# Kernel tuning notes

Measured on AMD Instinct MI355X. Metric: run time of the kernel, lower is better.

The kernel has to match this reference:

```python
import jax, jax.numpy as jnp
import numpy as np

# Constants from init_kwargs
DT = 0.01
NIV = 8          # energy_input_dim[1]
HID = 64         # hidden_dims[0]
FEAT = 501       # per-field microstructure feature length (501+501=1002)


def _lin(k, fin, fout):
    return jax.random.normal(k, (fin, fout), dtype=jnp.float32) / np.sqrt(fin)


def setup_inputs() -> dict:
    key = jax.random.key(0)
    ks = jax.random.split(key, 12)
    B, T = 8192, 512
    e = jax.random.normal(ks[0], (B, T, 1), dtype=jnp.float32) * 0.1
    e_dot = jax.random.normal(ks[1], (B, T, 1), dtype=jnp.float32) * 0.1
    # positive microstructure fields (code computes nu**-1 and E/nu**2)
    E = jax.random.uniform(ks[2], (B, FEAT), minval=0.5, maxval=2.0, dtype=jnp.float32)
    nu = jax.random.uniform(ks[3], (B, FEAT), minval=0.5, maxval=2.0, dtype=jnp.float32)
    return {
        "e": e, "e_dot": e_dot, "E": E, "nu": nu,
        # EnergyFunction.B : Linear(1002,64) -> ReLU -> Linear(64,niv)
        "Bw1": _lin(ks[4], 2 * FEAT, HID), "Bb1": jnp.zeros((HID,), jnp.float32),
        "Bw2": _lin(ks[5], HID, NIV), "Bb2": jnp.zeros((NIV,), jnp.float32),
        # InverseDissipationPotential.beta : Linear(1002,64)->Softplus->Linear(64,niv)->Softplus
        "bw1": _lin(ks[6], 2 * FEAT, HID), "bb1": jnp.zeros((HID,), jnp.float32),
        "bw2": _lin(ks[7], HID, NIV), "bb2": jnp.zeros((NIV,), jnp.float32),
    }


def reference(e, e_dot, E, nu, Bw1, Bb1, Bw2, Bb2, bw1, bb1, bw2, bb2):
    # --- microstructure encoder (TrueFeatures) ---
    nu_p = 1.0 / jnp.mean(1.0 / nu, axis=1, keepdims=True)                 # [B,1]
    E_p = jnp.mean(E / nu ** 2, axis=1, keepdims=True) * nu_p ** 2         # [B,1]
    m = jnp.concatenate([E, nu], axis=-1)                                  # [B,1002]

    # Time-invariant MLP coefficients (hoisted out of the time loop)
    Bm = jax.nn.relu(m @ Bw1 + Bb1) @ Bw2 + Bb2                            # [B,NIV]
    beta = jax.nn.softplus(jax.nn.softplus(m @ bw1 + bb1) @ bw2 + bb2)     # [B,NIV]
    Bsum = jnp.sum(Bm, axis=-1, keepdims=True)                             # [B,1]

    B_, niv = Bm.shape
    xi0 = jnp.zeros((B_, niv), dtype=e.dtype)

    def step(xi, inp):
        u, p = inp                                                          # [B,1],[B,1]
        # Analytic gradients of L = sum_{b,k} Bm_bk * (0.5*E' u^2 + 0.5*(u-xi_k)^2 + 0.5*sum_j xi_j^2)
        du = u - xi                                                         # [B,NIV]
        grad_u = Bsum * E_p * u + jnp.sum(Bm * du, axis=-1, keepdims=True)  # [B,1] (s_eq)
        grad_v = -Bm * du + Bsum * xi                                       # [B,NIV] (d)
        q = -grad_v
        # Analytic gradients of potential = -0.5*nu' p^2 + 0.5*sum(beta*q^2)
        grad_p = -nu_p * p                                                  # [B,1] (s_neq)
        grad_q = beta * q                                                   # [B,NIV] (kinetics)
        stress = grad_u - grad_p
        return xi + DT * grad_q, (stress, xi)

    xs = (jnp.swapaxes(e, 0, 1), jnp.swapaxes(e_dot, 0, 1))                 # [T,B,1]
    _, (stress_t, xi_t) = jax.lax.scan(step, xi0, xs)
    stress = jnp.swapaxes(stress_t, 0, 1)                                   # [B,T,1]
    xi = jnp.swapaxes(xi_t, 0, 1)                                           # [B,T,NIV]
    return stress, xi
```

## Files before the change

kernel.cpp:

```cpp
#include <hip/hip_runtime.h>
#include <hip/hip_bf16.h>

#define FEATN 501
#define KPAD 1024
#define MSTRIDE 1032
#define NB 8192
#define NT 512
#define DTC 0.01f

typedef __attribute__((ext_vector_type(8))) short short8;
typedef __attribute__((ext_vector_type(4))) short short4v;
typedef __attribute__((ext_vector_type(4))) float f32x4;

__device__ __forceinline__ float softplus_f(float x) {
    return fmaxf(x, 0.f) + log1pf(expf(-fabsf(x)));
}
__device__ __forceinline__ ushort f2bf(float x) {
    __hip_bfloat16 h = __float2bfloat16(x);
    return *reinterpret_cast<ushort*>(&h);
}
__device__ __forceinline__ void gl_lds16(const void* g, void* l) {
    __builtin_amdgcn_global_load_lds(
        (const __attribute__((address_space(1))) void*)g,
        (__attribute__((address_space(3))) void*)l, 16, 0, 0);
}
__device__ __forceinline__ float dpp_add(float x, const int ctrl) {
    int s = __builtin_bit_cast(int, x);
    int y;
    switch (ctrl) {
    case 0xB1:  y = __builtin_amdgcn_update_dpp(0, s, 0xB1, 0xf, 0xf, true); break;
    case 0x4E:  y = __builtin_amdgcn_update_dpp(0, s, 0x4E, 0xf, 0xf, true); break;
    default:    y = __builtin_amdgcn_update_dpp(0, s, 0x141, 0xf, 0xf, true); break;
    }
    return x + __builtin_bit_cast(float, y);
}

__global__ __launch_bounds__(256) void wtrans_kernel(
    const float* __restrict__ Bw1, const float* __restrict__ bw1,
    ushort* __restrict__ Wt) {
    const int h = blockIdx.x;
    const int lane = threadIdx.x & 63;
    const int wv = threadIdx.x >> 6;
    const float* W = (h < 64) ? Bw1 : bw1;
    const int col = h & 63;
    #pragma unroll
    for (int it = 0; it < 4; ++it) {
        const int k = it * 256 + wv * 64 + lane;
        const int ksrc = (k < FEATN) ? k
                       : (k >= 512 && k < 512 + FEATN) ? k - 11 : -1;
        const float v = (ksrc >= 0) ? W[(size_t)ksrc * 64 + col] : 0.f;
        Wt[(size_t)h * KPAD + k] = f2bf(v);
    }
}

__global__ __launch_bounds__(256) void enc_kernel(
    const float* __restrict__ E, const float* __restrict__ nu,
    const ushort* __restrict__ Wt,
    const float* __restrict__ Bb1, const float* __restrict__ bb1,
    const float* __restrict__ Bw2, const float* __restrict__ Bb2,
    const float* __restrict__ bw2, const float* __restrict__ bb2,
    float* __restrict__ xi) {
    __shared__ ushort Ml[16 * MSTRIDE];
    __shared__ float hid[128][17];
    __shared__ float nups[16], Eps[16];

    const int tid = threadIdx.x;
    const int wv = tid >> 6, lane = tid & 63;
    const int bb0 = blockIdx.x * 16;

    {
        const int bl = tid >> 4;
        const int t16 = tid & 15;
        const size_t base = (size_t)(bb0 + bl) * FEATN;
        float s1 = 0.f, s2 = 0.f;
        #pragma unroll
        for (int it = 0; it < 8; ++it) {
            const int i0 = it * 64 + t16 * 4;
            if (i0 + 3 < FEATN) {
                const float4 Ev = *(const float4*)(E + base + i0);
                const float4 nv = *(const float4*)(nu + base + i0);
                const float i0v = 1.0f / nv.x, i1v = 1.0f / nv.y;
                const float i2v = 1.0f / nv.z, i3v = 1.0f / nv.w;
                s1 += (i0v + i1v) + (i2v + i3v);
                s2 = fmaf(Ev.x, i0v * i0v, s2);
                s2 = fmaf(Ev.y, i1v * i1v, s2);
                s2 = fmaf(Ev.z, i2v * i2v, s2);
                s2 = fmaf(Ev.w, i3v * i3v, s2);
                short4v ep = {(short)f2bf(Ev.x), (short)f2bf(Ev.y),
                              (short)f2bf(Ev.z), (short)f2bf(Ev.w)};
                short4v np_ = {(short)f2bf(nv.x), (short)f2bf(nv.y),
                               (short)f2bf(nv.z), (short)f2bf(nv.w)};
                *(short4v*)&Ml[bl * MSTRIDE + i0] = ep;
                *(short4v*)&Ml[bl * MSTRIDE + 512 + i0] = np_;
            } else if (i0 < FEATN) {
                const float Ev = E[base + i0];
                const float nv = nu[base + i0];
                const float iv = 1.0f / nv;
                s1 += iv;
                s2 = fmaf(Ev, iv * iv, s2);
                Ml[bl * MSTRIDE + i0] = f2bf(Ev);
                Ml[bl * MSTRIDE + 512 + i0] = f2bf(nv);
            }
        }
        if (t16 < 11) {
            Ml[bl * MSTRIDE + FEATN + t16] = 0;
            Ml[bl * MSTRIDE + 512 + FEATN + t16] = 0;
        }
        #pragma unroll
        for (int o = 1; o < 16; o <<= 1) {
            s1 += __shfl_xor(s1, o);
            s2 += __shfl_xor(s2, o);
        }
        if (t16 == 0) {
            const float np = (float)FEATN / s1;
            nups[bl] = np;
            Eps[bl] = (s2 / (float)FEATN) * np * np;
        }
    }
    __syncthreads();

    const int r15 = lane & 15, kg = lane >> 4;
    const ushort* wp0 = Wt + (size_t)(wv * 32 + r15) * KPAD + kg * 8;
    const ushort* wp1 = wp0 + 16 * KPAD;
    const int boff = r15 * MSTRIDE + kg * 8;

    f32x4 acc0 = {0.f, 0.f, 0.f, 0.f}, acc1 = acc0;
    #pragma unroll 4
    for (int s = 0; s < 32; ++s) {
        const int kb = s * 32;
        const short8 a0 = *(const short8*)(wp0 + kb);
        const short8 a1 = *(const short8*)(wp1 + kb);
        const short8 b = *(const short8*)&Ml[boff + kb];
        acc0 = __builtin_amdgcn_mfma_f32_16x16x32_bf16(a0, b, acc0, 0, 0, 0);
        acc1 = __builtin_amdgcn_mfma_f32_16x16x32_bf16(a1, b, acc1, 0, 0, 0);
    }

    #pragma unroll
    for (int t = 0; t < 2; ++t) {
        #pragma unroll
        for (int r = 0; r < 4; ++r) {
            const int h = wv * 32 + t * 16 + kg * 4 + r;
            const float bias = (h < 64) ? Bb1[h] : bb1[h - 64];
            float v = (t ? acc1[r] : acc0[r]) + bias;
            v = (h < 64) ? fmaxf(v, 0.f) : softplus_f(v);
            hid[h][r15] = v;
        }
    }
    __syncthreads();

    if (tid < 128) {
        const int bl = tid >> 3, k = tid & 7;
        float dB = 0.f, db = 0.f;
        #pragma unroll 8
        for (int h = 0; h < 64; ++h) {
            dB = fmaf(hid[h][bl], Bw2[h * 8 + k], dB);
            db = fmaf(hid[64 + h][bl], bw2[h * 8 + k], db);
        }
        const float Bm = dB + Bb2[k];
        const float be = softplus_f(db + bb2[k]);
        float Bs = Bm;
        Bs += __shfl_xor(Bs, 1);
        Bs += __shfl_xor(Bs, 2);
        Bs += __shfl_xor(Bs, 4);
        float* cb = xi + (size_t)(bb0 + bl) * 4096;
        cb[k] = 1.f - DTC * be * (Bm + Bs);
        cb[8 + k] = DTC * be * Bm;
        cb[16 + k] = Bm;
        if (k == 0) { cb[24] = Bs * Eps[bl]; cb[25] = nups[bl]; }
    }
}

__global__ __launch_bounds__(256) void time_kernel(
    const float* __restrict__ e, const float* __restrict__ ed,
    const float* coef, float* stress, float* xi_out) {
    __shared__ float els[4][512];
    __shared__ float pls[4][512];
    __shared__ float scr[4][256];
    const int wv = threadIdx.x >> 6;
    const int wid = (blockIdx.x << 2) + wv;
    const int lane = threadIdx.x & 63;
    const int j = lane >> 3, k = lane & 7;

    const float* eb = e + (size_t)wid * NT;
    const float* edb = ed + (size_t)wid * NT;
    gl_lds16(eb + lane * 4, &els[wv][0]);
    gl_lds16(eb + 256 + lane * 4, &els[wv][256]);
    gl_lds16(edb + lane * 4, &pls[wv][0]);
    gl_lds16(edb + 256 + lane * 4, &pls[wv][256]);

    const float* cb = coef + (size_t)wid * 4096;
    const float a = cb[k];
    const float c = cb[8 + k];
    const float Bm = cb[16 + k];
    const float sE = cb[24];
    const float nup = cb[25];
    asm volatile("s_waitcnt vmcnt(0)" ::: "memory");

    const float a2 = a * a, a4 = a2 * a2;
    float A = 1.f;
    if (j & 1) A *= a;
    if (j & 2) A *= a2;
    if (j & 4) A *= a4;
    float pw[8];
    {
        float run = c;
        #pragma unroll
        for (int i = 7; i >= 0; --i) {
            const bool on = (i < j);
            pw[i] = on ? run : 0.f;
            run = on ? run * a : run;
        }
    }

    float* xb = xi_out + (size_t)wid * (NT * 8);
    float* sb = stress + (size_t)wid * NT;
    const float* el = &els[wv][0];
    const float* pl = &pls[wv][0];

    float4 q0 = *(const float4*)(el);
    float4 q1 = *(const float4*)(el + 4);
    float uj = el[j];
    float pj = pl[j];

    float xs = 0.f;
    for (int g = 0; g < 16; ++g) {
        const int T0 = g * 32;
        float vx[4], sv[4];
        #pragma unroll
        for (int w = 0; w < 4; ++w) {
            const int t0 = T0 + w * 8;
            const float u0 = q0.x, u1 = q0.y, u2 = q0.z, u3 = q0.w;
            const float u4 = q1.x, u5 = q1.y, u6 = q1.z, u7 = q1.w;
            const float cuj = uj, cpj = pj;
            if (t0 + 8 < NT) {
                q0 = *(const float4*)(el + t0 + 8);
                q1 = *(const float4*)(el + t0 + 12);
                uj = el[t0 + 8 + j];
                pj = pl[t0 + 8 + j];
            }
            float xi_j = A * xs;
            xi_j = fmaf(pw[0], u0, xi_j);
            xi_j = fmaf(pw[1], u1, xi_j);
            xi_j = fmaf(pw[2], u2, xi_j);
            xi_j = fmaf(pw[3], u3, xi_j);
            xi_j = fmaf(pw[4], u4, xi_j);
            xi_j = fmaf(pw[5], u5, xi_j);
            xi_j = fmaf(pw[6], u6, xi_j);
            xi_j = fmaf(pw[7], u7, xi_j);
            vx[w] = xi_j;
            float r = Bm * (cuj - xi_j);
            r = dpp_add(r, 0xB1);
            r = dpp_add(r, 0x4E);
            r = dpp_add(r, 0x141);
            sv[w] = fmaf(sE, cuj, fmaf(nup, cpj, r));
            xs = fmaf(a, __shfl(xi_j, 56 + k), c * u7);
        }
        #pragma unroll
        for (int w = 0; w < 4; ++w) scr[wv][w * 64 + lane] = vx[w];
        *(float4*)(xb + T0 * 8 + lane * 4) =
            *(const float4*)&scr[wv][lane * 4];
        if (k == 0) {
            #pragma unroll
            for (int w = 0; w < 4; ++w) scr[wv][w * 8 + j] = sv[w];
        }
        if (lane < 8)
            *(float4*)(sb + T0 + lane * 4) =
                *(const float4*)&scr[wv][lane * 4];
    }
}

extern "C" void kernel_launch(void* const* d_in, const int* in_sizes, int n_in,
                              void* d_out, int out_size, void* d_ws, size_t ws_size,
                              hipStream_t stream) {
    const float* e   = (const float*)d_in[0];
    const float* ed  = (const float*)d_in[1];
    const float* E   = (const float*)d_in[2];
    const float* nu  = (const float*)d_in[3];
    const float* Bw1 = (const float*)d_in[4];
    const float* Bb1 = (const float*)d_in[5];
    const float* Bw2 = (const float*)d_in[6];
    const float* Bb2 = (const float*)d_in[7];
    const float* bw1 = (const float*)d_in[8];
    const float* bb1 = (const float*)d_in[9];
    const float* bw2 = (const float*)d_in[10];
    const float* bb2 = (const float*)d_in[11];

    float* out = (float*)d_out;
    float* stress = out;
    float* xi = out + (size_t)NB * NT;
    ushort* Wt = (ushort*)out;

    wtrans_kernel<<<128, 256, 0, stream>>>(Bw1, bw1, Wt);
    enc_kernel<<<512, 256, 0, stream>>>(E, nu, Wt, Bb1, bb1,
                                        Bw2, Bb2, bw2, bb2, xi);
    time_kernel<<<2048, 256, 0, stream>>>(e, ed, xi, stress, xi);
}
```

Baseline: 69.35 us.

## Split encoder K reduction across four wave groups with 1024-thread blocks

Result: faster. 67.23 us (-3.1%).

```diff
diff --git a/kernel.cpp b/kernel.cpp
--- a/kernel.cpp
+++ b/kernel.cpp
@@ -53,7 +53,7 @@
     }
 }
 
-__global__ __launch_bounds__(256) void enc_kernel(
+__global__ __launch_bounds__(1024, 8) void enc_kernel(
     const float* __restrict__ E, const float* __restrict__ nu,
     const ushort* __restrict__ Wt,
     const float* __restrict__ Bb1, const float* __restrict__ bb1,
@@ -61,21 +61,21 @@
     const float* __restrict__ bw2, const float* __restrict__ bb2,
     float* __restrict__ xi) {
     __shared__ ushort Ml[16 * MSTRIDE];
+    __shared__ float red[3][2048];
     __shared__ float hid[128][17];
     __shared__ float nups[16], Eps[16];
 
     const int tid = threadIdx.x;
-    const int wv = tid >> 6, lane = tid & 63;
+    const int w = tid >> 6, lane = tid & 63;
     const int bb0 = blockIdx.x * 16;
 
     {
-        const int bl = tid >> 4;
-        const int t16 = tid & 15;
+        const int bl = w;
         const size_t base = (size_t)(bb0 + bl) * FEATN;
         float s1 = 0.f, s2 = 0.f;
         #pragma unroll
-        for (int it = 0; it < 8; ++it) {
-            const int i0 = it * 64 + t16 * 4;
+        for (int it = 0; it < 2; ++it) {
+            const int i0 = it * 256 + lane * 4;
             if (i0 + 3 < FEATN) {
                 const float4 Ev = *(const float4*)(E + base + i0);
                 const float4 nv = *(const float4*)(nu + base + i0);
@@ -102,16 +102,16 @@
                 Ml[bl * MSTRIDE + 512 + i0] = f2bf(nv);
             }
         }
-        if (t16 < 11) {
-            Ml[bl * MSTRIDE + FEATN + t16] = 0;
-            Ml[bl * MSTRIDE + 512 + FEATN + t16] = 0;
-        }
-        #pragma unroll
-        for (int o = 1; o < 16; o <<= 1) {
+        if (lane < 11) {
+            Ml[bl * MSTRIDE + FEATN + lane] = 0;
+            Ml[bl * MSTRIDE + 512 + FEATN + lane] = 0;
+        }
+        #pragma unroll
+        for (int o = 32; o; o >>= 1) {
             s1 += __shfl_xor(s1, o);
             s2 += __shfl_xor(s2, o);
         }
-        if (t16 == 0) {
+        if (lane == 0) {
             const float np = (float)FEATN / s1;
             nups[bl] = np;
             Eps[bl] = (s2 / (float)FEATN) * np * np;
@@ -119,14 +119,15 @@
     }
     __syncthreads();
 
+    const int g = w & 3, q = w >> 2;
     const int r15 = lane & 15, kg = lane >> 4;
-    const ushort* wp0 = Wt + (size_t)(wv * 32 + r15) * KPAD + kg * 8;
+    const ushort* wp0 = Wt + (size_t)(g * 32 + r15) * KPAD + q * 256 + kg * 8;
     const ushort* wp1 = wp0 + 16 * KPAD;
-    const int boff = r15 * MSTRIDE + kg * 8;
+    const int boff = r15 * MSTRIDE + q * 256 + kg * 8;
 
     f32x4 acc0 = {0.f, 0.f, 0.f, 0.f}, acc1 = acc0;
-    #pragma unroll 4
-    for (int s = 0; s < 32; ++s) {
+    #pragma unroll
+    for (int s = 0; s < 8; ++s) {
         const int kb = s * 32;
         const short8 a0 = *(const short8*)(wp0 + kb);
         const short8 a1 = *(const short8*)(wp1 + kb);
@@ -135,15 +136,27 @@
         acc1 = __builtin_amdgcn_mfma_f32_16x16x32_bf16(a1, b, acc1, 0, 0, 0);
     }
 
-    #pragma unroll
-    for (int t = 0; t < 2; ++t) {
-        #pragma unroll
-        for (int r = 0; r < 4; ++r) {
-            const int h = wv * 32 + t * 16 + kg * 4 + r;
-            const float bias = (h < 64) ? Bb1[h] : bb1[h - 64];
-            float v = (t ? acc1[r] : acc0[r]) + bias;
-            v = (h < 64) ? fmaxf(v, 0.f) : softplus_f(v);
-            hid[h][r15] = v;
+    if (q > 0) {
+        *(f32x4*)&red[q - 1][(g * 64 + lane) * 8] = acc0;
+        *(f32x4*)&red[q - 1][(g * 64 + lane) * 8 + 4] = acc1;
+    }
+    __syncthreads();
+    if (q == 0) {
+        #pragma unroll
+        for (int p = 0; p < 3; ++p) {
+            acc0 += *(const f32x4*)&red[p][(g * 64 + lane) * 8];
+            acc1 += *(const f32x4*)&red[p][(g * 64 + lane) * 8 + 4];
+        }
+        #pragma unroll
+        for (int t = 0; t < 2; ++t) {
+            #pragma unroll
+            for (int r = 0; r < 4; ++r) {
+                const int h = g * 32 + t * 16 + kg * 4 + r;
+                const float bias = (h < 64) ? Bb1[h] : bb1[h - 64];
+                float v = (t ? acc1[r] : acc0[r]) + bias;
+                v = (h < 64) ? fmaxf(v, 0.f) : softplus_f(v);
+                hid[h][r15] = v;
+            }
         }
     }
     __syncthreads();
@@ -291,7 +304,7 @@
     ushort* Wt = (ushort*)out;
 
     wtrans_kernel<<<128, 256, 0, stream>>>(Bw1, bw1, Wt);
-    enc_kernel<<<512, 256, 0, stream>>>(E, nu, Wt, Bb1, bb1,
-                                        Bw2, Bb2, bw2, bb2, xi);
+    enc_kernel<<<512, 1024, 0, stream>>>(E, nu, Wt, Bb1, bb1,
+                                         Bw2, Bb2, bw2, bb2, xi);
     time_kernel<<<2048, 256, 0, stream>>>(e, ed, xi, stress, xi);
 }
```
